# Kernel optimization log

Hardware: AMD Instinct MI355X
Metric: run time of the kernel (lower is better)

Reference implementation:

```python
import jax, jax.numpy as jnp
import numpy as np

# Paul Kellet pink-noise filter coefficients (verbatim from the torch source)
_A = np.array([0.99886, 0.99332, 0.969, 0.8665, 0.55, -0.7616], dtype=np.float32)   # pole feedback
_C = np.array([0.0555179, 0.0750759, 0.153852, 0.3104856, 0.5329522, -0.016898], dtype=np.float32)  # input gains
_B6_GAIN = 0.115926   # b6 is the previous white sample scaled (one-sample delay)
_DIRECT = 0.5362      # direct white feedthrough
_OUT_GAIN = 0.11


def setup_inputs() -> dict:
    key = jax.random.key(0)
    B, L = 256, 65536
    white = jax.random.normal(key, (B, L), dtype=jnp.float32)
    return {"white": white}


def reference(white):
    """Pink noise via the 6-pole IIR recurrence from SignalGenerator.noise('pink'),
    vectorized over a batch of channels; sequential time handled by lax.scan.
    white: [B, L] -> pink: [B, L]
    """
    B, L = white.shape
    a = jnp.asarray(_A)  # [6]
    c = jnp.asarray(_C)  # [6]

    def step(carry, w_t):
        # carry: (b [B,6] pole states, b6 [B] delayed-white state); w_t: [B]
        b, b6 = carry
        b = a * b + w_t[:, None] * c                      # [B,6]
        pink_t = (b.sum(-1) + b6 + _DIRECT * w_t) * _OUT_GAIN  # [B]
        return (b, _B6_GAIN * w_t), pink_t

    init = (jnp.zeros((B, 6), dtype=white.dtype), jnp.zeros((B,), dtype=white.dtype))
    _, pink_tb = jax.lax.scan(step, init, white.T)  # scan over time: [L, B]
    return pink_tb.T  # [B, L]
```

## Files before the change

### kernel.cpp

```cpp
#include <hip/hip_runtime.h>


constexpr int kL = 65536;
constexpr int kThr = 512;
constexpr int kWaves = kThr / 64;
constexpr int kT = 8192;
constexpr int kW = 8192;
constexpr int kSpan = kT + kW;
constexpr int kPT = kSpan / kThr;
constexpr int kLd = kSpan / 4 / kThr;
constexpr int kSt = kT / 4 / kThr;
constexpr int kTilesPerCh = kL / kT;

__device__ __forceinline__ int swz(int i) {
    return i ^ (((i >> 5) & 7) << 2);
}

__global__ __launch_bounds__(kThr, 2) void pink_tile(
    const float* __restrict__ white, float* __restrict__ pink)
{
    constexpr float A[6] = {0.99886f, 0.99332f, 0.969f, 0.8665f, 0.55f, -0.7616f};
    constexpr float C[6] = {0.0555179f, 0.0750759f, 0.153852f, 0.3104856f, 0.5329522f, -0.016898f};
    constexpr float B6G = 0.115926f, DIRECT = 0.5362f, OUTG = 0.11f;

    __shared__ __align__(16) float buf[kSpan];
    __shared__ float swv[6][kWaves];

    const int tid = threadIdx.x, lane = tid & 63, wave = tid >> 6;
    const int ch = blockIdx.x / kTilesPerCh;
    const int tI = blockIdx.x % kTilesPerCh;
    const size_t outBase = (size_t)ch * kL + (size_t)tI * kT;

    const float4* src4 = (const float4*)(white + outBase) - (kW / 4);
    float4 v[kLd];
    #pragma unroll
    for (int k = 0; k < kLd; ++k) {
        const int j = tid + k * kThr;
        if (tI != 0 || k >= kLd / 2) v[k] = src4[j];
        else                         v[k] = make_float4(0.f, 0.f, 0.f, 0.f);
    }
    #pragma unroll
    for (int k = 0; k < kLd; ++k)
        *(float4*)&buf[swz(4 * (tid + k * kThr))] = v[k];

    float mPT[6], pmL[6], Mwv[6];
    #pragma unroll
    for (int p = 0; p < 6; ++p) {
        float q = A[p];
        #pragma unroll
        for (int i = 0; i < 5; ++i) q *= q;
        mPT[p] = q;
        float pm = 1.f, qq = q;
        #pragma unroll
        for (int b = 0; b < 6; ++b) { if ((lane >> b) & 1) pm *= qq; qq *= qq; }
        pmL[p] = pm;
        Mwv[p] = qq;
    }
    __syncthreads();

    const float pwl = (tid == 0) ? 0.f : buf[swz(kPT * tid - 1)];

    float e[6] = {0.f, 0.f, 0.f, 0.f, 0.f, 0.f};
    #pragma unroll
    for (int kk = 0; kk < kPT / 4; ++kk) {
        const float4 x = *(const float4*)&buf[swz(kPT * tid + 4 * kk)];
        const float* xp = &x.x;
        #pragma unroll
        for (int j = 0; j < 4; ++j) {
            const float ww = xp[j];
            #pragma unroll
            for (int p = 0; p < 6; ++p) e[p] = fmaf(A[p], e[p], ww * C[p]);
        }
    }

    float mk[6];
    #pragma unroll
    for (int p = 0; p < 6; ++p) mk[p] = mPT[p];
    #pragma unroll
    for (int r = 0; r < 6; ++r) {
        const int off = 1 << r;
        float fe[6];
        #pragma unroll
        for (int p = 0; p < 6; ++p) fe[p] = __shfl_up(e[p], off);
        if (lane >= off) {
            #pragma unroll
            for (int p = 0; p < 6; ++p) e[p] = fmaf(mk[p], fe[p], e[p]);
        }
        #pragma unroll
        for (int p = 0; p < 6; ++p) mk[p] *= mk[p];
    }
    float ex[6];
    #pragma unroll
    for (int p = 0; p < 6; ++p) {
        ex[p] = __shfl_up(e[p], 1);
        if (lane == 0) ex[p] = 0.f;
    }
    if (lane == 63) {
        #pragma unroll
        for (int p = 0; p < 6; ++p) swv[p][wave] = e[p];
    }
    __syncthreads();

    float b[6];
    #pragma unroll
    for (int p = 0; p < 6; ++p) {
        float X = 0.f;
        #pragma unroll
        for (int w2 = 0; w2 < kWaves; ++w2)
            if (w2 < wave) X = fmaf(Mwv[p], X, swv[p][w2]);
        b[p] = fmaf(pmL[p], X, ex[p]);
    }

    if (tid >= kThr / 2) {
        float b6 = B6G * pwl;
        #pragma unroll
        for (int kk = 0; kk < kPT / 4; ++kk) {
            const float4 x = *(const float4*)&buf[swz(kPT * tid + 4 * kk)];
            const float* xp = &x.x;
            float4 o;
            float* op = &o.x;
            #pragma unroll
            for (int j = 0; j < 4; ++j) {
                const float ww = xp[j];
                #pragma unroll
                for (int p = 0; p < 6; ++p) b[p] = fmaf(A[p], b[p], ww * C[p]);
                const float sum = ((b[0]+b[1]) + (b[2]+b[3])) + ((b[4]+b[5]) + b6);
                op[j] = fmaf(DIRECT, ww, sum) * OUTG;
                b6 = B6G * ww;
            }
            *(float4*)&buf[swz(kPT * tid + 4 * kk)] = o;
        }
    }
    __syncthreads();

    float4* dst4 = (float4*)(pink + outBase);
    #pragma unroll
    for (int k = 0; k < kSt; ++k)
        dst4[tid + k * kThr] =
            *(const float4*)&buf[swz(kW + 4 * (tid + k * kThr))];
}

extern "C" void kernel_launch(void* const* d_in, const int* in_sizes, int n_in,
                              void* d_out, int out_size, void* d_ws, size_t ws_size,
                              hipStream_t stream) {
    const float* white = (const float*)d_in[0];
    float* pink = (float*)d_out;
    const int nCh = in_sizes[0] / kL;
    const int nBlk = nCh * kTilesPerCh;

    hipLaunchKernelGGL(pink_tile, dim3(nBlk), dim3(kThr), 0, stream,
                       white, pink);
}
```

Measured before the change: 122.9 us.

## Read warmup window directly from global, halve LDS tile, raise occupancy

The first half of the threads now read the warmup (look-back) window straight from global memory and run their filter partial sums in registers. Only the second half stage the output tile into LDS. This halves shared memory per block from 64KB to 32KB and raises the launch bound to 3 blocks per CU. The cost is uncoalesced per-thread strided global reads of 128 bytes for the warmup half, plus extra LDS work for the tile half.

```diff
diff --git a/kernel.cpp b/kernel.cpp
--- a/kernel.cpp
+++ b/kernel.cpp
@@ -4,44 +4,30 @@
 constexpr int kL = 65536;
 constexpr int kThr = 512;
 constexpr int kWaves = kThr / 64;
+constexpr int kHalf = kThr / 2;
 constexpr int kT = 8192;
 constexpr int kW = 8192;
-constexpr int kSpan = kT + kW;
-constexpr int kPT = kSpan / kThr;
-constexpr int kLd = kSpan / 4 / kThr;
-constexpr int kSt = kT / 4 / kThr;
+constexpr int kPT = 32;
 constexpr int kTilesPerCh = kL / kT;
 
 __device__ __forceinline__ int swz(int i) {
     return i ^ (((i >> 5) & 7) << 2);
 }
 
-__global__ __launch_bounds__(kThr, 2) void pink_tile(
+__global__ __launch_bounds__(kThr, 3) void pink_tile(
     const float* __restrict__ white, float* __restrict__ pink)
 {
     constexpr float A[6] = {0.99886f, 0.99332f, 0.969f, 0.8665f, 0.55f, -0.7616f};
     constexpr float C[6] = {0.0555179f, 0.0750759f, 0.153852f, 0.3104856f, 0.5329522f, -0.016898f};
     constexpr float B6G = 0.115926f, DIRECT = 0.5362f, OUTG = 0.11f;
 
-    __shared__ __align__(16) float buf[kSpan];
+    __shared__ __align__(16) float buf[kT];
     __shared__ float swv[6][kWaves];
 
     const int tid = threadIdx.x, lane = tid & 63, wave = tid >> 6;
     const int ch = blockIdx.x / kTilesPerCh;
     const int tI = blockIdx.x % kTilesPerCh;
     const size_t outBase = (size_t)ch * kL + (size_t)tI * kT;
-
-    const float4* src4 = (const float4*)(white + outBase) - (kW / 4);
-    float4 v[kLd];
-    #pragma unroll
-    for (int k = 0; k < kLd; ++k) {
-        const int j = tid + k * kThr;
-        if (tI != 0 || k >= kLd / 2) v[k] = src4[j];
-        else                         v[k] = make_float4(0.f, 0.f, 0.f, 0.f);
-    }
-    #pragma unroll
-    for (int k = 0; k < kLd; ++k)
-        *(float4*)&buf[swz(4 * (tid + k * kThr))] = v[k];
 
     float mPT[6], pmL[6], Mwv[6];
     #pragma unroll
@@ -56,21 +42,55 @@
         pmL[p] = pm;
         Mwv[p] = qq;
     }
+
+    float e[6] = {0.f, 0.f, 0.f, 0.f, 0.f, 0.f};
+
+    if (tid < kHalf) {
+        if (tI != 0) {
+            const float* g = white + outBase - kW + (size_t)kPT * tid;
+            #pragma unroll
+            for (int kk = 0; kk < kPT / 4; ++kk) {
+                const float4 x = *(const float4*)(g + 4 * kk);
+                const float* xp = &x.x;
+                #pragma unroll
+                for (int j = 0; j < 4; ++j) {
+                    const float ww = xp[j];
+                    #pragma unroll
+                    for (int p = 0; p < 6; ++p) e[p] = fmaf(A[p], e[p], ww * C[p]);
+                }
+            }
+        }
+    } else {
+        const int u = tid - kHalf;
+        const float4* src4 = (const float4*)(white + outBase);
+        #pragma unroll
+        for (int g2 = 0; g2 < 2; ++g2) {
+            float4 v[4];
+            #pragma unroll
+            for (int k = 0; k < 4; ++k) v[k] = src4[u + (g2 * 4 + k) * kHalf];
+            #pragma unroll
+            for (int k = 0; k < 4; ++k)
+                *(float4*)&buf[swz(4 * (u + (g2 * 4 + k) * kHalf))] = v[k];
+        }
+    }
     __syncthreads();
 
-    const float pwl = (tid == 0) ? 0.f : buf[swz(kPT * tid - 1)];
-
-    float e[6] = {0.f, 0.f, 0.f, 0.f, 0.f, 0.f};
-    #pragma unroll
-    for (int kk = 0; kk < kPT / 4; ++kk) {
-        const float4 x = *(const float4*)&buf[swz(kPT * tid + 4 * kk)];
-        const float* xp = &x.x;
+    float pwl = 0.f;
+    if (tid >= kHalf) {
+        const int u = tid - kHalf;
         #pragma unroll
-        for (int j = 0; j < 4; ++j) {
-            const float ww = xp[j];
+        for (int kk = 0; kk < kPT / 4; ++kk) {
+            const float4 x = *(const float4*)&buf[swz(kPT * u + 4 * kk)];
+            const float* xp = &x.x;
             #pragma unroll
-            for (int p = 0; p < 6; ++p) e[p] = fmaf(A[p], e[p], ww * C[p]);
+            for (int j = 0; j < 4; ++j) {
+                const float ww = xp[j];
+                #pragma unroll
+                for (int p = 0; p < 6; ++p) e[p] = fmaf(A[p], e[p], ww * C[p]);
+            }
         }
+        if (u == 0) pwl = (tI != 0) ? white[outBase - 1] : 0.f;
+        else        pwl = buf[swz(kPT * u - 1)];
     }
 
     float mk[6];
@@ -101,21 +121,21 @@
     }
     __syncthreads();
 
-    float b[6];
-    #pragma unroll
-    for (int p = 0; p < 6; ++p) {
-        float X = 0.f;
+    if (tid >= kHalf) {
+        const int u = tid - kHalf;
+        float b[6];
         #pragma unroll
-        for (int w2 = 0; w2 < kWaves; ++w2)
-            if (w2 < wave) X = fmaf(Mwv[p], X, swv[p][w2]);
-        b[p] = fmaf(pmL[p], X, ex[p]);
-    }
-
-    if (tid >= kThr / 2) {
+        for (int p = 0; p < 6; ++p) {
+            float X = 0.f;
+            #pragma unroll
+            for (int w2 = 0; w2 < kWaves; ++w2)
+                if (w2 < wave) X = fmaf(Mwv[p], X, swv[p][w2]);
+            b[p] = fmaf(pmL[p], X, ex[p]);
+        }
         float b6 = B6G * pwl;
         #pragma unroll
         for (int kk = 0; kk < kPT / 4; ++kk) {
-            const float4 x = *(const float4*)&buf[swz(kPT * tid + 4 * kk)];
+            const float4 x = *(const float4*)&buf[swz(kPT * u + 4 * kk)];
             const float* xp = &x.x;
             float4 o;
             float* op = &o.x;
@@ -128,16 +148,15 @@
                 op[j] = fmaf(DIRECT, ww, sum) * OUTG;
                 b6 = B6G * ww;
             }
-            *(float4*)&buf[swz(kPT * tid + 4 * kk)] = o;
+            *(float4*)&buf[swz(kPT * u + 4 * kk)] = o;
         }
     }
     __syncthreads();
 
     float4* dst4 = (float4*)(pink + outBase);
     #pragma unroll
-    for (int k = 0; k < kSt; ++k)
-        dst4[tid + k * kThr] =
-            *(const float4*)&buf[swz(kW + 4 * (tid + k * kThr))];
+    for (int k = 0; k < 4; ++k)
+        dst4[tid + k * kThr] = *(const float4*)&buf[swz(4 * (tid + k * kThr))];
 }
 
 extern "C" void kernel_launch(void* const* d_in, const int* in_sizes, int n_in,
```

Measured after the change: 127.4 us. +3.7%, slower.

## Process warmup window and tile in parallel per thread, all threads emit output

Applied to the files above, without the earlier changes.

Before, each thread scanned 32 samples across a 16K span of warmup plus tile, and only the upper half of threads produced output. Now each thread scans 16 samples of the warmup window and 16 of the tile as two independent chains. The warmup reduction is folded into a carry-in for the tile, and every thread writes output. The C gains are factored out of the recurrence and applied once in the output sum, which saves a multiply per pole per sample. The aim is to halve the serial chain length per thread and use every thread in the final pass, at the cost of more registers and extra shuffles.

```diff
diff --git a/kernel.cpp b/kernel.cpp
--- a/kernel.cpp
+++ b/kernel.cpp
@@ -6,10 +6,7 @@
 constexpr int kWaves = kThr / 64;
 constexpr int kT = 8192;
 constexpr int kW = 8192;
-constexpr int kSpan = kT + kW;
-constexpr int kPT = kSpan / kThr;
-constexpr int kLd = kSpan / 4 / kThr;
-constexpr int kSt = kT / 4 / kThr;
+constexpr int kPT = kT / kThr;
 constexpr int kTilesPerCh = kL / kT;
 
 __device__ __forceinline__ int swz(int i) {
@@ -23,32 +20,46 @@
     constexpr float C[6] = {0.0555179f, 0.0750759f, 0.153852f, 0.3104856f, 0.5329522f, -0.016898f};
     constexpr float B6G = 0.115926f, DIRECT = 0.5362f, OUTG = 0.11f;
 
-    __shared__ __align__(16) float buf[kSpan];
-    __shared__ float swv[6][kWaves];
+    __shared__ __align__(16) float bufA[kW];
+    __shared__ __align__(16) float bufB[kT];
+    __shared__ float swvA[6][kWaves];
+    __shared__ float swvB[6][kWaves];
 
     const int tid = threadIdx.x, lane = tid & 63, wave = tid >> 6;
     const int ch = blockIdx.x / kTilesPerCh;
     const int tI = blockIdx.x % kTilesPerCh;
     const size_t outBase = (size_t)ch * kL + (size_t)tI * kT;
 
-    const float4* src4 = (const float4*)(white + outBase) - (kW / 4);
-    float4 v[kLd];
-    #pragma unroll
-    for (int k = 0; k < kLd; ++k) {
-        const int j = tid + k * kThr;
-        if (tI != 0 || k >= kLd / 2) v[k] = src4[j];
-        else                         v[k] = make_float4(0.f, 0.f, 0.f, 0.f);
+    const float4* sB = (const float4*)(white + outBase);
+    if (tI != 0) {
+        const float4* sA = (const float4*)(white + outBase - kW);
+        float4 a0 = sA[tid], a1 = sA[tid + kThr],
+               a2 = sA[tid + 2*kThr], a3 = sA[tid + 3*kThr];
+        float4 b0 = sB[tid], b1 = sB[tid + kThr],
+               b2 = sB[tid + 2*kThr], b3 = sB[tid + 3*kThr];
+        *(float4*)&bufA[swz(4*tid)]             = a0;
+        *(float4*)&bufA[swz(4*(tid + kThr))]    = a1;
+        *(float4*)&bufA[swz(4*(tid + 2*kThr))]  = a2;
+        *(float4*)&bufA[swz(4*(tid + 3*kThr))]  = a3;
+        *(float4*)&bufB[swz(4*tid)]             = b0;
+        *(float4*)&bufB[swz(4*(tid + kThr))]    = b1;
+        *(float4*)&bufB[swz(4*(tid + 2*kThr))]  = b2;
+        *(float4*)&bufB[swz(4*(tid + 3*kThr))]  = b3;
+    } else {
+        float4 b0 = sB[tid], b1 = sB[tid + kThr],
+               b2 = sB[tid + 2*kThr], b3 = sB[tid + 3*kThr];
+        *(float4*)&bufB[swz(4*tid)]             = b0;
+        *(float4*)&bufB[swz(4*(tid + kThr))]    = b1;
+        *(float4*)&bufB[swz(4*(tid + 2*kThr))]  = b2;
+        *(float4*)&bufB[swz(4*(tid + 3*kThr))]  = b3;
     }
-    #pragma unroll
-    for (int k = 0; k < kLd; ++k)
-        *(float4*)&buf[swz(4 * (tid + k * kThr))] = v[k];
 
     float mPT[6], pmL[6], Mwv[6];
     #pragma unroll
     for (int p = 0; p < 6; ++p) {
         float q = A[p];
         #pragma unroll
-        for (int i = 0; i < 5; ++i) q *= q;
+        for (int i = 0; i < 4; ++i) q *= q;
         mPT[p] = q;
         float pm = 1.f, qq = q;
         #pragma unroll
@@ -58,20 +69,30 @@
     }
     __syncthreads();
 
-    const float pwl = (tid == 0) ? 0.f : buf[swz(kPT * tid - 1)];
-
-    float e[6] = {0.f, 0.f, 0.f, 0.f, 0.f, 0.f};
+    float eA[6] = {0.f,0.f,0.f,0.f,0.f,0.f};
+    float eB[6] = {0.f,0.f,0.f,0.f,0.f,0.f};
     #pragma unroll
     for (int kk = 0; kk < kPT / 4; ++kk) {
-        const float4 x = *(const float4*)&buf[swz(kPT * tid + 4 * kk)];
-        const float* xp = &x.x;
+        float4 xA;
+        if (tI != 0) xA = *(const float4*)&bufA[swz(kPT * tid + 4 * kk)];
+        const float4 xB = *(const float4*)&bufB[swz(kPT * tid + 4 * kk)];
+        const float* ap = &xA.x;
+        const float* bp = &xB.x;
         #pragma unroll
         for (int j = 0; j < 4; ++j) {
-            const float ww = xp[j];
+            if (tI != 0) {
+                const float wa = ap[j];
+                #pragma unroll
+                for (int p = 0; p < 6; ++p) eA[p] = fmaf(A[p], eA[p], wa);
+            }
+            const float wb = bp[j];
             #pragma unroll
-            for (int p = 0; p < 6; ++p) e[p] = fmaf(A[p], e[p], ww * C[p]);
+            for (int p = 0; p < 6; ++p) eB[p] = fmaf(A[p], eB[p], wb);
         }
     }
+    const float pwl = (tid == 0)
+        ? ((tI != 0) ? bufA[swz(kW - 1)] : 0.f)
+        : bufB[swz(kPT * tid - 1)];
 
     float mk[6];
     #pragma unroll
@@ -79,12 +100,14 @@
     #pragma unroll
     for (int r = 0; r < 6; ++r) {
         const int off = 1 << r;
-        float fe[6];
+        float fA[6], fB[6];
         #pragma unroll
-        for (int p = 0; p < 6; ++p) fe[p] = __shfl_up(e[p], off);
+        for (int p = 0; p < 6; ++p) { fA[p] = __shfl_up(eA[p], off);
+                                      fB[p] = __shfl_up(eB[p], off); }
         if (lane >= off) {
             #pragma unroll
-            for (int p = 0; p < 6; ++p) e[p] = fmaf(mk[p], fe[p], e[p]);
+            for (int p = 0; p < 6; ++p) { eA[p] = fmaf(mk[p], fA[p], eA[p]);
+                                          eB[p] = fmaf(mk[p], fB[p], eB[p]); }
         }
         #pragma unroll
         for (int p = 0; p < 6; ++p) mk[p] *= mk[p];
@@ -92,52 +115,59 @@
     float ex[6];
     #pragma unroll
     for (int p = 0; p < 6; ++p) {
-        ex[p] = __shfl_up(e[p], 1);
+        ex[p] = __shfl_up(eB[p], 1);
         if (lane == 0) ex[p] = 0.f;
     }
     if (lane == 63) {
         #pragma unroll
-        for (int p = 0; p < 6; ++p) swv[p][wave] = e[p];
+        for (int p = 0; p < 6; ++p) { swvA[p][wave] = eA[p];
+                                      swvB[p][wave] = eB[p]; }
     }
     __syncthreads();
 
     float b[6];
     #pragma unroll
     for (int p = 0; p < 6; ++p) {
-        float X = 0.f;
+        float R = 0.f;
+        if (tI != 0) {
+            #pragma unroll
+            for (int w2 = 0; w2 < kWaves; ++w2)
+                R = fmaf(Mwv[p], R, swvA[p][w2]);
+        }
+        float X = R;
         #pragma unroll
         for (int w2 = 0; w2 < kWaves; ++w2)
-            if (w2 < wave) X = fmaf(Mwv[p], X, swv[p][w2]);
+            if (w2 < wave) X = fmaf(Mwv[p], X, swvB[p][w2]);
         b[p] = fmaf(pmL[p], X, ex[p]);
     }
+    float b6 = B6G * pwl;
 
-    if (tid >= kThr / 2) {
-        float b6 = B6G * pwl;
+    #pragma unroll
+    for (int kk = 0; kk < kPT / 4; ++kk) {
+        const float4 x = *(const float4*)&bufB[swz(kPT * tid + 4 * kk)];
+        const float* xp = &x.x;
+        float4 o;
+        float* op = &o.x;
         #pragma unroll
-        for (int kk = 0; kk < kPT / 4; ++kk) {
-            const float4 x = *(const float4*)&buf[swz(kPT * tid + 4 * kk)];
-            const float* xp = &x.x;
-            float4 o;
-            float* op = &o.x;
+        for (int j = 0; j < 4; ++j) {
+            const float ww = xp[j];
             #pragma unroll
-            for (int j = 0; j < 4; ++j) {
-                const float ww = xp[j];
-                #pragma unroll
-                for (int p = 0; p < 6; ++p) b[p] = fmaf(A[p], b[p], ww * C[p]);
-                const float sum = ((b[0]+b[1]) + (b[2]+b[3])) + ((b[4]+b[5]) + b6);
-                op[j] = fmaf(DIRECT, ww, sum) * OUTG;
-                b6 = B6G * ww;
-            }
-            *(float4*)&buf[swz(kPT * tid + 4 * kk)] = o;
+            for (int p = 0; p < 6; ++p) b[p] = fmaf(A[p], b[p], ww);
+            float t0 = C[0] * b[0];  t0 = fmaf(C[1], b[1], t0);
+            float t1 = C[2] * b[2];  t1 = fmaf(C[3], b[3], t1);
+            float t2 = C[4] * b[4];  t2 = fmaf(C[5], b[5], t2);
+            const float sum = (t0 + t1) + (t2 + b6);
+            op[j] = fmaf(DIRECT, ww, sum) * OUTG;
+            b6 = B6G * ww;
         }
+        *(float4*)&bufB[swz(kPT * tid + 4 * kk)] = o;
     }
     __syncthreads();
 
     float4* dst4 = (float4*)(pink + outBase);
     #pragma unroll
-    for (int k = 0; k < kSt; ++k)
-        dst4[tid + k * kThr] =
-            *(const float4*)&buf[swz(kW + 4 * (tid + k * kThr))];
+    for (int k = 0; k < 4; ++k)
+        dst4[tid + k * kThr] = *(const float4*)&bufB[swz(4 * (tid + k * kThr))];
 }
 
 extern "C" void kernel_launch(void* const* d_in, const int* in_sizes, int n_in,
```

Result: slower. 128.5 us (+4.6%).
